# Optimization experiments

Hardware: AMD Instinct MI355X
Metric: run time of the kernel (lower is better)

## Reference

```python
import jax, jax.numpy as jnp
import numpy as np

LR = 0.001       # ISTA step size (default in _IstaStep)
GAMMA = 0.1      # lambdav sparsity penalty (gamma init kwarg)
N_STEPS = 10     # number of unrolled ISTA iterations


def _soft_threshold(x, t):
    # _proxOp: max(x - t, 0) + min(x + t, 0)
    return jnp.maximum(x - t, 0.0) + jnp.minimum(x + t, 0.0)


def setup_inputs() -> dict:
    key = jax.random.key(0)
    k1, k2 = jax.random.split(key)
    B, I, O = 131072, 128, 256
    inputs = jax.random.normal(k1, (B, I), dtype=jnp.float32)
    # glorot_uniform for W of shape (output_dim, input_dim)
    scale = float(np.sqrt(6.0 / (O + I)))
    W = jax.random.uniform(k2, (O, I), dtype=jnp.float32, minval=-scale, maxval=scale)
    return {"inputs": inputs, "W": W}


def reference(inputs, W):
    # inputs: [B, I]; W: [O, I]; states x: [B, O]
    B = inputs.shape[0]
    O = W.shape[0]
    x0 = jnp.zeros((B, O), dtype=inputs.dtype)

    def step(x, _):
        recon = x @ W                              # [B, I], linear activation
        # analytic grad of sum((inputs - recon)^2) w.r.t. x (what T.grad computes)
        grad = 2.0 * (recon - inputs) @ W.T        # [B, O]
        new_x = _soft_threshold(x - LR * grad, LR * GAMMA)
        # theano.gradient.disconnected_grad on the new state each step
        new_x = jax.lax.stop_gradient(new_x)
        return new_x, None

    x_final, _ = jax.lax.scan(step, x0, None, length=N_STEPS)
    # return_reconstruction=True -> dot(outs, W)
    return x_final @ W
```

## Files before the change

kernel.cpp:

```cpp
#include <hip/hip_runtime.h>
#include <hip/hip_bf16.h>

typedef __attribute__((ext_vector_type(4))) float  f32x4;
typedef __attribute__((ext_vector_type(16))) float f32x16;
typedef __attribute__((ext_vector_type(8))) short  s16x8;
typedef __attribute__((ext_vector_type(4))) short  s16x4;

#define THR_  1.0e-4f
#define SC_   2.0e-3f

__device__ __forceinline__ unsigned short f2bf(float f) {
  union { __hip_bfloat16 b; unsigned short u; } cv;
  cv.b = __float2bfloat16(f);
  return cv.u;
}

__device__ __forceinline__ float sthr(float v) {
  return v - fmaxf(fminf(v, THR_), -THR_);
}

__global__ void sc_prep(const float* __restrict__ W, unsigned short* __restrict__ ws) {
  const int b = blockIdx.x;
  const int l = threadIdx.x;
  const int r = l & 31, h = l >> 5;
  if (b < 128) {
    const int kc = b >> 3, ntg = b & 7;
    const int n = ntg * 32 + r;
    const int k0 = kc * 16 + 8 * h;
    float s[8];
    #pragma unroll
    for (int j = 0; j < 8; ++j) s[j] = 0.0f;
    for (int i = 0; i < 128; ++i) {
      const float wn = W[n * 128 + i];
      #pragma unroll
      for (int j = 0; j < 8; ++j) s[j] += W[(k0 + j) * 128 + i] * wn;
    }
    unsigned short* dst = ws + ((unsigned)b * 64u + l) * 8u;
    #pragma unroll
    for (int j = 0; j < 8; ++j) dst[j] = f2bf(-SC_ * s[j]);
  } else if (b < 192) {
    const int bb = b - 128;
    const int kc = bb >> 3, ntg = bb & 7;
    const int n = ntg * 32 + r;
    const int k0 = kc * 16 + 8 * h;
    unsigned short* dst = ws + 65536u + ((unsigned)bb * 64u + l) * 8u;
    #pragma unroll
    for (int j = 0; j < 8; ++j) dst[j] = f2bf(SC_ * W[n * 128 + k0 + j]);
  } else {
    const int bb = b - 192;
    const int kc = bb >> 2, it = bb & 3;
    const int i = it * 32 + r;
    const int n0 = kc * 16 + 8 * h;
    unsigned short* dst = ws + 98304u + ((unsigned)bb * 64u + l) * 8u;
    #pragma unroll
    for (int j = 0; j < 8; ++j) dst[j] = f2bf(W[(n0 + j) * 128 + i]);
  }
}

__global__ __launch_bounds__(256, 2) void sc_fused(
    const float* __restrict__ inp,
    const unsigned short* __restrict__ wsp,
    float* __restrict__ outp)
{
  __shared__ __align__(16) unsigned char lds[33280];

  if ((blockIdx.x >> 8) & 1) {
    __builtin_amdgcn_s_sleep(15);
    __builtin_amdgcn_s_sleep(5);
  }

  const int tid = threadIdx.x;
  const int l = tid & 63;
  const int w = tid >> 6;
  const int h = l >> 5;
  const int r31 = l & 31;
  const long row0 = (long)blockIdx.x * 32;

  const int rB0 = r31 * 520 + h * 16;
  const int rB1 = rB0 + 16640;
  const int wB0 = r31 * 520 + h * 8 + w * 128;
  const int wB1 = wB0 + 16640;

  #pragma unroll
  for (int rep = 0; rep < 4; ++rep) {
    const int flat = rep * 256 + tid;
    const int rr = flat >> 5;
    const int c4 = flat & 31;
    const f32x4 v = *reinterpret_cast<const f32x4*>(inp + (row0 + rr) * 128 + c4 * 4);
    s16x4 p;
    p[0] = (short)f2bf(v[0]); p[1] = (short)f2bf(v[1]);
    p[2] = (short)f2bf(v[2]); p[3] = (short)f2bf(v[3]);
    *reinterpret_cast<s16x4*>(lds + 16640 + rr * 264 + c4 * 8) = p;
  }

  s16x8 gfr[32];
  #pragma unroll
  for (int kc = 0; kc < 8; ++kc)
    #pragma unroll
    for (int nt = 0; nt < 2; ++nt)
      gfr[kc * 2 + nt] = *reinterpret_cast<const s16x8*>(
          wsp + 65536u + ((unsigned)(kc * 8 + w * 2 + nt) * 64u + l) * 8u);

  __syncthreads();

  f32x16 accA[2], accB[2], creg[2];
  #pragma unroll
  for (int nt = 0; nt < 2; ++nt)
    #pragma unroll
    for (int e = 0; e < 16; ++e) { accA[nt][e] = 0.0f; accB[nt][e] = 0.0f; }

  const int ib = 16640 + r31 * 264 + h * 16;
  #pragma unroll
  for (int kc = 0; kc < 4; ++kc) {
    const s16x8 bA = *reinterpret_cast<const s16x8*>(lds + ib + kc * 32);
    const s16x8 bB = *reinterpret_cast<const s16x8*>(lds + ib + (kc + 4) * 32);
    __builtin_amdgcn_s_setprio(1);
    #pragma unroll
    for (int nt = 0; nt < 2; ++nt)
      accA[nt] = __builtin_amdgcn_mfma_f32_32x32x16_bf16(gfr[kc * 2 + nt], bA, accA[nt], 0, 0, 0);
    #pragma unroll
    for (int nt = 0; nt < 2; ++nt)
      accB[nt] = __builtin_amdgcn_mfma_f32_32x32x16_bf16(gfr[(kc + 4) * 2 + nt], bB, accB[nt], 0, 0, 0);
    __builtin_amdgcn_s_setprio(0);
  }

  #pragma unroll
  for (int nt = 0; nt < 2; ++nt)
    #pragma unroll
    for (int q = 0; q < 4; ++q) {
      float f0 = accA[nt][4 * q + 0] + accB[nt][4 * q + 0];
      float f1 = accA[nt][4 * q + 1] + accB[nt][4 * q + 1];
      float f2 = accA[nt][4 * q + 2] + accB[nt][4 * q + 2];
      float f3 = accA[nt][4 * q + 3] + accB[nt][4 * q + 3];
      creg[nt][4 * q + 0] = f0; creg[nt][4 * q + 1] = f1;
      creg[nt][4 * q + 2] = f2; creg[nt][4 * q + 3] = f3;
      f0 = sthr(f0); f1 = sthr(f1); f2 = sthr(f2); f3 = sthr(f3);
      s16x4 p;
      p[0] = (short)f2bf(f0); p[1] = (short)f2bf(f1);
      p[2] = (short)f2bf(f2); p[3] = (short)f2bf(f3);
      *reinterpret_cast<s16x4*>(lds + wB0 + nt * 64 + q * 16) = p;
      accA[nt][4 * q + 0] = f0 + creg[nt][4 * q + 0];
      accA[nt][4 * q + 1] = f1 + creg[nt][4 * q + 1];
      accA[nt][4 * q + 2] = f2 + creg[nt][4 * q + 2];
      accA[nt][4 * q + 3] = f3 + creg[nt][4 * q + 3];
      accB[nt][4 * q + 0] = 0.0f; accB[nt][4 * q + 1] = 0.0f;
      accB[nt][4 * q + 2] = 0.0f; accB[nt][4 * q + 3] = 0.0f;
    }

  #pragma unroll
  for (int kc = 0; kc < 16; ++kc)
    #pragma unroll
    for (int nt = 0; nt < 2; ++nt)
      gfr[kc * 2 + nt] = *reinterpret_cast<const s16x8*>(
          wsp + ((unsigned)(kc * 8 + w * 2 + nt) * 64u + l) * 8u);

  auto STEP = [&](const int rb, const int wb) {
    __syncthreads();
    #pragma unroll
    for (int kc = 0; kc < 8; ++kc) {
      const s16x8 bA = *reinterpret_cast<const s16x8*>(lds + rb + kc * 32);
      const s16x8 bB = *reinterpret_cast<const s16x8*>(lds + rb + (kc + 8) * 32);
      __builtin_amdgcn_s_setprio(1);
      #pragma unroll
      for (int nt = 0; nt < 2; ++nt)
        accA[nt] = __builtin_amdgcn_mfma_f32_32x32x16_bf16(gfr[kc * 2 + nt], bA, accA[nt], 0, 0, 0);
      #pragma unroll
      for (int nt = 0; nt < 2; ++nt)
        accB[nt] = __builtin_amdgcn_mfma_f32_32x32x16_bf16(gfr[(kc + 8) * 2 + nt], bB, accB[nt], 0, 0, 0);
      __builtin_amdgcn_s_setprio(0);
    }
    #pragma unroll
    for (int nt = 0; nt < 2; ++nt)
      #pragma unroll
      for (int q = 0; q < 4; ++q) {
        float f0 = sthr(accA[nt][4 * q + 0] + accB[nt][4 * q + 0]);
        float f1 = sthr(accA[nt][4 * q + 1] + accB[nt][4 * q + 1]);
        float f2 = sthr(accA[nt][4 * q + 2] + accB[nt][4 * q + 2]);
        float f3 = sthr(accA[nt][4 * q + 3] + accB[nt][4 * q + 3]);
        s16x4 p;
        p[0] = (short)f2bf(f0); p[1] = (short)f2bf(f1);
        p[2] = (short)f2bf(f2); p[3] = (short)f2bf(f3);
        *reinterpret_cast<s16x4*>(lds + wb + nt * 64 + q * 16) = p;
        accA[nt][4 * q + 0] = f0 + creg[nt][4 * q + 0];
        accA[nt][4 * q + 1] = f1 + creg[nt][4 * q + 1];
        accA[nt][4 * q + 2] = f2 + creg[nt][4 * q + 2];
        accA[nt][4 * q + 3] = f3 + creg[nt][4 * q + 3];
        accB[nt][4 * q + 0] = 0.0f; accB[nt][4 * q + 1] = 0.0f;
        accB[nt][4 * q + 2] = 0.0f; accB[nt][4 * q + 3] = 0.0f;
      }
  };

  #pragma unroll 1
  for (int p = 0; p < 4; ++p) {
    STEP(rB0, wB1);
    STEP(rB1, wB0);
  }
  STEP(rB0, wB1);

  __syncthreads();
  #pragma unroll
  for (int kc = 0; kc < 16; ++kc)
    gfr[kc] = *reinterpret_cast<const s16x8*>(
        wsp + 98304u + ((unsigned)(kc * 4 + w) * 64u + l) * 8u);
  f32x16 oA, oB;
  #pragma unroll
  for (int e = 0; e < 16; ++e) { oA[e] = 0.0f; oB[e] = 0.0f; }
  #pragma unroll
  for (int kc = 0; kc < 8; ++kc) {
    const s16x8 bA = *reinterpret_cast<const s16x8*>(lds + rB1 + kc * 32);
    const s16x8 bB = *reinterpret_cast<const s16x8*>(lds + rB1 + (kc + 8) * 32);
    __builtin_amdgcn_s_setprio(1);
    oA = __builtin_amdgcn_mfma_f32_32x32x16_bf16(gfr[kc], bA, oA, 0, 0, 0);
    oB = __builtin_amdgcn_mfma_f32_32x32x16_bf16(gfr[kc + 8], bB, oB, 0, 0, 0);
    __builtin_amdgcn_s_setprio(0);
  }
  const int ob = r31 * 520 + h * 16 + w * 128;
  #pragma unroll
  for (int q = 0; q < 4; ++q) {
    f32x4 p;
    p[0] = oA[4 * q + 0] + oB[4 * q + 0]; p[1] = oA[4 * q + 1] + oB[4 * q + 1];
    p[2] = oA[4 * q + 2] + oB[4 * q + 2]; p[3] = oA[4 * q + 3] + oB[4 * q + 3];
    *reinterpret_cast<f32x4*>(lds + ob + q * 32) = p;
  }
  __syncthreads();
  #pragma unroll
  for (int rep = 0; rep < 4; ++rep) {
    const int flat = rep * 256 + tid;
    const int rr = flat >> 5;
    const int c4 = flat & 31;
    const f32x4 v = *reinterpret_cast<const f32x4*>(lds + rr * 520 + c4 * 16);
    *reinterpret_cast<f32x4*>(outp + (row0 + rr) * 128 + c4 * 4) = v;
  }
}

extern "C" void kernel_launch(void* const* d_in, const int* in_sizes, int n_in,
                              void* d_out, int out_size, void* d_ws, size_t ws_size,
                              hipStream_t stream) {
  const float* inp = (const float*)d_in[0];
  const float* W   = (const float*)d_in[1];
  unsigned short* ws = (unsigned short*)d_ws;
  float* outp = (float*)d_out;
  const int B = in_sizes[0] / 128;
  sc_prep<<<256, 64, 0, stream>>>(W, ws);
  sc_fused<<<B / 32, 256, 0, stream>>>(inp, ws, outp);
}
```

Measured before the change: 179.7 us.

## Ping-pong two wave groups so MFMA and soft-threshold epilogue overlap

Each block now handles 64 rows with 512 threads split into two 4-wave groups. While one group runs the MFMA step on its 32-row tile, the other runs its threshold and writeback, and the roles swap at each barrier. The goal is to hide the VALU/LDS epilogue behind matrix-core work instead of relying on two independent blocks and a sleep-based stagger. The constant term is now kept as packed bf16 instead of fp32 registers, which lowers register pressure but adds rounding error to the per-step bias.

```diff
diff --git a/kernel.cpp b/kernel.cpp
--- a/kernel.cpp
+++ b/kernel.cpp
@@ -14,9 +14,14 @@
   cv.b = __float2bfloat16(f);
   return cv.u;
 }
-
 __device__ __forceinline__ float sthr(float v) {
   return v - fmaxf(fminf(v, THR_), -THR_);
+}
+__device__ __forceinline__ float bflo(unsigned u) {
+  return __builtin_bit_cast(float, u << 16);
+}
+__device__ __forceinline__ float bfhi(unsigned u) {
+  return __builtin_bit_cast(float, u & 0xffff0000u);
 }
 
 __global__ void sc_prep(const float* __restrict__ W, unsigned short* __restrict__ ws) {
@@ -57,40 +62,39 @@
   }
 }
 
-__global__ __launch_bounds__(256, 2) void sc_fused(
+__global__ __launch_bounds__(512, 2) void sc_fused(
     const float* __restrict__ inp,
     const unsigned short* __restrict__ wsp,
     float* __restrict__ outp)
 {
-  __shared__ __align__(16) unsigned char lds[33280];
-
-  if ((blockIdx.x >> 8) & 1) {
-    __builtin_amdgcn_s_sleep(15);
-    __builtin_amdgcn_s_sleep(5);
-  }
+  __shared__ __align__(16) unsigned char lds[66560];
 
   const int tid = threadIdx.x;
   const int l = tid & 63;
-  const int w = tid >> 6;
+  const int wv = tid >> 6;
+  const int grp = wv >> 2;
+  const int w4 = wv & 3;
   const int h = l >> 5;
   const int r31 = l & 31;
-  const long row0 = (long)blockIdx.x * 32;
-
-  const int rB0 = r31 * 520 + h * 16;
-  const int rB1 = rB0 + 16640;
-  const int wB0 = r31 * 520 + h * 8 + w * 128;
-  const int wB1 = wB0 + 16640;
+  const long row0 = (long)blockIdx.x * 64;
+
+  const int XA = grp * 33280;
+  const int XB = XA + 16640;
+
+  const int rB = r31 * 520 + h * 16;
+  const int wB = r31 * 520 + h * 8 + w4 * 128;
 
   #pragma unroll
   for (int rep = 0; rep < 4; ++rep) {
-    const int flat = rep * 256 + tid;
+    const int flat = rep * 512 + tid;
     const int rr = flat >> 5;
     const int c4 = flat & 31;
     const f32x4 v = *reinterpret_cast<const f32x4*>(inp + (row0 + rr) * 128 + c4 * 4);
     s16x4 p;
     p[0] = (short)f2bf(v[0]); p[1] = (short)f2bf(v[1]);
     p[2] = (short)f2bf(v[2]); p[3] = (short)f2bf(v[3]);
-    *reinterpret_cast<s16x4*>(lds + 16640 + rr * 264 + c4 * 8) = p;
+    const int base = 16640 + (rr >> 5) * 33280 + (rr & 31) * 264;
+    *reinterpret_cast<s16x4*>(lds + base + c4 * 8) = p;
   }
 
   s16x8 gfr[32];
@@ -99,17 +103,17 @@
     #pragma unroll
     for (int nt = 0; nt < 2; ++nt)
       gfr[kc * 2 + nt] = *reinterpret_cast<const s16x8*>(
-          wsp + 65536u + ((unsigned)(kc * 8 + w * 2 + nt) * 64u + l) * 8u);
-
-  __syncthreads();
-
-  f32x16 accA[2], accB[2], creg[2];
+          wsp + 65536u + ((unsigned)(kc * 8 + w4 * 2 + nt) * 64u + l) * 8u);
+
+  __syncthreads();
+
+  f32x16 accA[2], accB[2];
   #pragma unroll
   for (int nt = 0; nt < 2; ++nt)
     #pragma unroll
     for (int e = 0; e < 16; ++e) { accA[nt][e] = 0.0f; accB[nt][e] = 0.0f; }
 
-  const int ib = 16640 + r31 * 264 + h * 16;
+  const int ib = XB + r31 * 264 + h * 16;
   #pragma unroll
   for (int kc = 0; kc < 4; ++kc) {
     const s16x8 bA = *reinterpret_cast<const s16x8*>(lds + ib + kc * 32);
@@ -124,27 +128,16 @@
     __builtin_amdgcn_s_setprio(0);
   }
 
+  unsigned cp[16];
   #pragma unroll
   for (int nt = 0; nt < 2; ++nt)
     #pragma unroll
-    for (int q = 0; q < 4; ++q) {
-      float f0 = accA[nt][4 * q + 0] + accB[nt][4 * q + 0];
-      float f1 = accA[nt][4 * q + 1] + accB[nt][4 * q + 1];
-      float f2 = accA[nt][4 * q + 2] + accB[nt][4 * q + 2];
-      float f3 = accA[nt][4 * q + 3] + accB[nt][4 * q + 3];
-      creg[nt][4 * q + 0] = f0; creg[nt][4 * q + 1] = f1;
-      creg[nt][4 * q + 2] = f2; creg[nt][4 * q + 3] = f3;
-      f0 = sthr(f0); f1 = sthr(f1); f2 = sthr(f2); f3 = sthr(f3);
-      s16x4 p;
-      p[0] = (short)f2bf(f0); p[1] = (short)f2bf(f1);
-      p[2] = (short)f2bf(f2); p[3] = (short)f2bf(f3);
-      *reinterpret_cast<s16x4*>(lds + wB0 + nt * 64 + q * 16) = p;
-      accA[nt][4 * q + 0] = f0 + creg[nt][4 * q + 0];
-      accA[nt][4 * q + 1] = f1 + creg[nt][4 * q + 1];
-      accA[nt][4 * q + 2] = f2 + creg[nt][4 * q + 2];
-      accA[nt][4 * q + 3] = f3 + creg[nt][4 * q + 3];
-      accB[nt][4 * q + 0] = 0.0f; accB[nt][4 * q + 1] = 0.0f;
-      accB[nt][4 * q + 2] = 0.0f; accB[nt][4 * q + 3] = 0.0f;
+    for (int j = 0; j < 8; ++j) {
+      const float e0 = accA[nt][2 * j + 0] + accB[nt][2 * j + 0];
+      const float e1 = accA[nt][2 * j + 1] + accB[nt][2 * j + 1];
+      cp[nt * 8 + j] = (unsigned)f2bf(e0) | ((unsigned)f2bf(e1) << 16);
+      accA[nt][2 * j + 0] = e0; accA[nt][2 * j + 1] = e1;
+      accB[nt][2 * j + 0] = 0.0f; accB[nt][2 * j + 1] = 0.0f;
     }
 
   #pragma unroll
@@ -152,14 +145,13 @@
     #pragma unroll
     for (int nt = 0; nt < 2; ++nt)
       gfr[kc * 2 + nt] = *reinterpret_cast<const s16x8*>(
-          wsp + ((unsigned)(kc * 8 + w * 2 + nt) * 64u + l) * 8u);
-
-  auto STEP = [&](const int rb, const int wb) {
-    __syncthreads();
+          wsp + ((unsigned)(kc * 8 + w4 * 2 + nt) * 64u + l) * 8u);
+
+  auto MSTEP = [&](const int base) {
     #pragma unroll
     for (int kc = 0; kc < 8; ++kc) {
-      const s16x8 bA = *reinterpret_cast<const s16x8*>(lds + rb + kc * 32);
-      const s16x8 bB = *reinterpret_cast<const s16x8*>(lds + rb + (kc + 8) * 32);
+      const s16x8 bA = *reinterpret_cast<const s16x8*>(lds + base + rB + kc * 32);
+      const s16x8 bB = *reinterpret_cast<const s16x8*>(lds + base + rB + (kc + 8) * 32);
       __builtin_amdgcn_s_setprio(1);
       #pragma unroll
       for (int nt = 0; nt < 2; ++nt)
@@ -169,67 +161,116 @@
         accB[nt] = __builtin_amdgcn_mfma_f32_32x32x16_bf16(gfr[(kc + 8) * 2 + nt], bB, accB[nt], 0, 0, 0);
       __builtin_amdgcn_s_setprio(0);
     }
+  };
+  auto WB = [&](const int base) {
     #pragma unroll
     for (int nt = 0; nt < 2; ++nt)
       #pragma unroll
       for (int q = 0; q < 4; ++q) {
-        float f0 = sthr(accA[nt][4 * q + 0] + accB[nt][4 * q + 0]);
-        float f1 = sthr(accA[nt][4 * q + 1] + accB[nt][4 * q + 1]);
-        float f2 = sthr(accA[nt][4 * q + 2] + accB[nt][4 * q + 2]);
-        float f3 = sthr(accA[nt][4 * q + 3] + accB[nt][4 * q + 3]);
+        float x0 = sthr(accA[nt][4 * q + 0] + accB[nt][4 * q + 0]);
+        float x1 = sthr(accA[nt][4 * q + 1] + accB[nt][4 * q + 1]);
+        float x2 = sthr(accA[nt][4 * q + 2] + accB[nt][4 * q + 2]);
+        float x3 = sthr(accA[nt][4 * q + 3] + accB[nt][4 * q + 3]);
         s16x4 p;
-        p[0] = (short)f2bf(f0); p[1] = (short)f2bf(f1);
-        p[2] = (short)f2bf(f2); p[3] = (short)f2bf(f3);
-        *reinterpret_cast<s16x4*>(lds + wb + nt * 64 + q * 16) = p;
-        accA[nt][4 * q + 0] = f0 + creg[nt][4 * q + 0];
-        accA[nt][4 * q + 1] = f1 + creg[nt][4 * q + 1];
-        accA[nt][4 * q + 2] = f2 + creg[nt][4 * q + 2];
-        accA[nt][4 * q + 3] = f3 + creg[nt][4 * q + 3];
+        p[0] = (short)f2bf(x0); p[1] = (short)f2bf(x1);
+        p[2] = (short)f2bf(x2); p[3] = (short)f2bf(x3);
+        *reinterpret_cast<s16x4*>(lds + base + wB + nt * 64 + q * 16) = p;
+        const unsigned pa = cp[nt * 8 + q * 2], pb = cp[nt * 8 + q * 2 + 1];
+        accA[nt][4 * q + 0] = x0 + bflo(pa); accA[nt][4 * q + 1] = x1 + bfhi(pa);
+        accA[nt][4 * q + 2] = x2 + bflo(pb); accA[nt][4 * q + 3] = x3 + bfhi(pb);
         accB[nt][4 * q + 0] = 0.0f; accB[nt][4 * q + 1] = 0.0f;
         accB[nt][4 * q + 2] = 0.0f; accB[nt][4 * q + 3] = 0.0f;
       }
   };
 
+  if (!grp) WB(XA);
+  __syncthreads();
+
   #pragma unroll 1
-  for (int p = 0; p < 4; ++p) {
-    STEP(rB0, wB1);
-    STEP(rB1, wB0);
-  }
-  STEP(rB0, wB1);
-
-  __syncthreads();
-  #pragma unroll
-  for (int kc = 0; kc < 16; ++kc)
-    gfr[kc] = *reinterpret_cast<const s16x8*>(
-        wsp + 98304u + ((unsigned)(kc * 4 + w) * 64u + l) * 8u);
-  f32x16 oA, oB;
-  #pragma unroll
-  for (int e = 0; e < 16; ++e) { oA[e] = 0.0f; oB[e] = 0.0f; }
-  #pragma unroll
-  for (int kc = 0; kc < 8; ++kc) {
-    const s16x8 bA = *reinterpret_cast<const s16x8*>(lds + rB1 + kc * 32);
-    const s16x8 bB = *reinterpret_cast<const s16x8*>(lds + rB1 + (kc + 8) * 32);
+  for (int i = 0; i < 9; ++i) {
+    const int pa = XA + ((i & 1) ? 16640 : 0);
+    if (!grp) MSTEP(pa); else WB(pa);
+    __syncthreads();
+    if (!grp) WB(pa ^ 16640); else MSTEP(pa);
+    __syncthreads();
+  }
+
+  if (!grp) {
+    #pragma unroll
+    for (int kc = 0; kc < 16; ++kc)
+      gfr[kc] = *reinterpret_cast<const s16x8*>(
+          wsp + 98304u + ((unsigned)(kc * 4 + w4) * 64u + l) * 8u);
+    #pragma unroll
+    for (int e = 0; e < 16; ++e) { accA[0][e] = 0.0f; accB[0][e] = 0.0f; }
     __builtin_amdgcn_s_setprio(1);
-    oA = __builtin_amdgcn_mfma_f32_32x32x16_bf16(gfr[kc], bA, oA, 0, 0, 0);
-    oB = __builtin_amdgcn_mfma_f32_32x32x16_bf16(gfr[kc + 8], bB, oB, 0, 0, 0);
+    #pragma unroll
+    for (int kc = 0; kc < 8; ++kc) {
+      const s16x8 bA = *reinterpret_cast<const s16x8*>(lds + XB + rB + kc * 32);
+      const s16x8 bB = *reinterpret_cast<const s16x8*>(lds + XB + rB + (kc + 8) * 32);
+      accA[0] = __builtin_amdgcn_mfma_f32_32x32x16_bf16(gfr[kc], bA, accA[0], 0, 0, 0);
+      accB[0] = __builtin_amdgcn_mfma_f32_32x32x16_bf16(gfr[kc + 8], bB, accB[0], 0, 0, 0);
+    }
     __builtin_amdgcn_s_setprio(0);
-  }
-  const int ob = r31 * 520 + h * 16 + w * 128;
-  #pragma unroll
-  for (int q = 0; q < 4; ++q) {
-    f32x4 p;
-    p[0] = oA[4 * q + 0] + oB[4 * q + 0]; p[1] = oA[4 * q + 1] + oB[4 * q + 1];
-    p[2] = oA[4 * q + 2] + oB[4 * q + 2]; p[3] = oA[4 * q + 3] + oB[4 * q + 3];
-    *reinterpret_cast<f32x4*>(lds + ob + q * 32) = p;
-  }
-  __syncthreads();
-  #pragma unroll
-  for (int rep = 0; rep < 4; ++rep) {
-    const int flat = rep * 256 + tid;
+    const int ob = XA + r31 * 520 + w4 * 128 + h * 16;
+    #pragma unroll
+    for (int q = 0; q < 4; ++q) {
+      f32x4 p;
+      p[0] = accA[0][4 * q + 0] + accB[0][4 * q + 0];
+      p[1] = accA[0][4 * q + 1] + accB[0][4 * q + 1];
+      p[2] = accA[0][4 * q + 2] + accB[0][4 * q + 2];
+      p[3] = accA[0][4 * q + 3] + accB[0][4 * q + 3];
+      *reinterpret_cast<f32x4*>(lds + ob + q * 32) = p;
+    }
+  } else {
+    WB(XB);
+  }
+  __syncthreads();
+
+  if (grp) {
+    #pragma unroll
+    for (int kc = 0; kc < 16; ++kc)
+      gfr[kc] = *reinterpret_cast<const s16x8*>(
+          wsp + 98304u + ((unsigned)(kc * 4 + w4) * 64u + l) * 8u);
+    #pragma unroll
+    for (int e = 0; e < 16; ++e) { accA[0][e] = 0.0f; accB[0][e] = 0.0f; }
+    __builtin_amdgcn_s_setprio(1);
+    #pragma unroll
+    for (int kc = 0; kc < 8; ++kc) {
+      const s16x8 bA = *reinterpret_cast<const s16x8*>(lds + XB + rB + kc * 32);
+      const s16x8 bB = *reinterpret_cast<const s16x8*>(lds + XB + rB + (kc + 8) * 32);
+      accA[0] = __builtin_amdgcn_mfma_f32_32x32x16_bf16(gfr[kc], bA, accA[0], 0, 0, 0);
+      accB[0] = __builtin_amdgcn_mfma_f32_32x32x16_bf16(gfr[kc + 8], bB, accB[0], 0, 0, 0);
+    }
+    __builtin_amdgcn_s_setprio(0);
+    const int ob = XA + r31 * 520 + w4 * 128 + h * 16;
+    #pragma unroll
+    for (int q = 0; q < 4; ++q) {
+      f32x4 p;
+      p[0] = accA[0][4 * q + 0] + accB[0][4 * q + 0];
+      p[1] = accA[0][4 * q + 1] + accB[0][4 * q + 1];
+      p[2] = accA[0][4 * q + 2] + accB[0][4 * q + 2];
+      p[3] = accA[0][4 * q + 3] + accB[0][4 * q + 3];
+      *reinterpret_cast<f32x4*>(lds + ob + q * 32) = p;
+    }
+  } else {
+    #pragma unroll
+    for (int rep = 0; rep < 4; ++rep) {
+      const int flat = rep * 256 + tid;
+      const int rr = flat >> 5;
+      const int c4 = flat & 31;
+      const f32x4 v = *reinterpret_cast<const f32x4*>(lds + rr * 520 + c4 * 16);
+      *reinterpret_cast<f32x4*>(outp + (row0 + rr) * 128 + c4 * 4) = v;
+    }
+  }
+  __syncthreads();
+
+  #pragma unroll
+  for (int rep = 0; rep < 2; ++rep) {
+    const int flat = rep * 512 + tid;
     const int rr = flat >> 5;
     const int c4 = flat & 31;
-    const f32x4 v = *reinterpret_cast<const f32x4*>(lds + rr * 520 + c4 * 16);
-    *reinterpret_cast<f32x4*>(outp + (row0 + rr) * 128 + c4 * 4) = v;
+    const f32x4 v = *reinterpret_cast<const f32x4*>(lds + 33280 + rr * 520 + c4 * 16);
+    *reinterpret_cast<f32x4*>(outp + (row0 + 32 + rr) * 128 + c4 * 4) = v;
   }
 }
 
@@ -242,5 +283,5 @@
   float* outp = (float*)d_out;
   const int B = in_sizes[0] / 128;
   sc_prep<<<256, 64, 0, stream>>>(W, ws);
-  sc_fused<<<B / 32, 256, 0, stream>>>(inp, ws, outp);
-}
+  sc_fused<<<B / 64, 512, 0, stream>>>(inp, ws, outp);
+}
```

After: 219.2 us. 1.22x slower.
